# Kernel tuning notes

Measured on AMD Instinct MI355X. Metric: run time of the kernel, lower is better.

The kernel has to match this reference:

```python
import jax, jax.numpy as jnp
import numpy as np

N, D, E, EDGE_DIM, HID4 = 8192, 128, 262144, 50, 32


def setup_inputs() -> dict:
    key = jax.random.key(0)
    k = jax.random.split(key, 8)
    return {
        "mag": jax.random.uniform(k[0], (N, D), dtype=jnp.float32),
        "phase": jax.random.normal(k[1], (N, D), dtype=jnp.float32),
        "edge_index": jax.random.randint(k[2], (2, E), 0, N, dtype=jnp.int64),
        "rbf": jax.random.uniform(k[3], (E, EDGE_DIM), dtype=jnp.float32),
        "W1": jax.random.normal(k[4], (EDGE_DIM, HID4), dtype=jnp.float32) * 0.1,
        "b1": jnp.zeros((HID4,), dtype=jnp.float32),
        "W2": jax.random.normal(k[5], (HID4, 1), dtype=jnp.float32) * 0.1,
        "b2": jnp.zeros((1,), dtype=jnp.float32),
    }


def reference(mag, phase, edge_index, rbf, W1, b1, W2, b2):
    # score_ij = sum_d |z_i||z_j| cos(theta_i - theta_j) / sqrt(D)
    # cos(a-b) identity: = (mag*cos(phase)) @ (mag*cos(phase))^T + (mag*sin)@(mag*sin)^T
    scale = jnp.sqrt(jnp.asarray(mag.shape[-1], mag.dtype))
    a = mag * jnp.cos(phase)  # [N, D]
    b = mag * jnp.sin(phase)  # [N, D]
    scores = (a @ a.T + b @ b.T) / scale  # [N, N]
    # edge bias: Linear -> SiLU -> Linear -> scalar, scattered onto (i, j)
    h = jax.nn.silu(rbf @ W1 + b1)       # [E, HID4]
    bias = (h @ W2 + b2)[:, 0]           # [E]
    scores = scores.at[edge_index[0], edge_index[1]].add(bias)
    attn = jax.nn.softmax(scores, axis=1)  # softmax over keys j
    new_mag = attn @ mag
    new_phase = attn @ phase
    return new_mag, new_phase
```

## Files before the change

kernel.cpp:

```cpp
#include <hip/hip_runtime.h>
#include <hip/hip_bf16.h>

#define NN 8192
#define DD 128
#define DQK 256
#define EE 262144
#define EDGE_DIM 50
#define HID 32
#define CAP 96
#define SCALE 0.08838834764831845f
#define SCALE_LOG2E 0.12752455522410585f

using f32x4 = __attribute__((ext_vector_type(4))) float;
using f32x2 = __attribute__((ext_vector_type(2))) float;
using bf16x8 = __attribute__((ext_vector_type(8))) short;
using s16x4 = __attribute__((ext_vector_type(4))) short;

static __device__ __forceinline__ short f2b(float f) {
  __hip_bfloat16 h = __float2bfloat16(f);
  return __builtin_bit_cast(short, h);
}
static __device__ __forceinline__ float b2f(short s) {
  unsigned u = ((unsigned)(unsigned short)s) << 16;
  return __builtin_bit_cast(float, u);
}
static __device__ __forceinline__ void gll(const short* g, short* l) {
  __builtin_amdgcn_global_load_lds(
      (const __attribute__((address_space(1))) void*)g,
      (__attribute__((address_space(3))) void*)l, 16, 0, 0);
}

__global__ __launch_bounds__(256) void k1_mega(
    const float* __restrict__ mag, const float* __restrict__ phase,
    short* __restrict__ qkb, short* __restrict__ vtb, short* __restrict__ vb16,
    const float* __restrict__ rbf, const float* __restrict__ W1,
    const float* __restrict__ b1, const float* __restrict__ W2,
    const float* __restrict__ b2, const int* __restrict__ eidx,
    float* __restrict__ bias, int* __restrict__ cnt, int* __restrict__ slot) {
  __shared__ float tile[64][65];
  int b = blockIdx.x;
  int tid = threadIdx.x;
  if (b < 4096) {
    int t = b * 256 + tid;
    int n = t >> 7, d = t & 127;
    float m = mag[t], p = phase[t];
    float sn, cs;
    __sincosf(p, &sn, &cs);
    qkb[(size_t)n * DQK + d] = f2b(m * cs);
    qkb[(size_t)n * DQK + 128 + d] = f2b(m * sn);
    vb16[(size_t)n * DQK + d] = f2b(m);
    vb16[(size_t)n * DQK + 128 + d] = f2b(p);
    return;
  }
  if (b < 4608) {
    int r = b - 4096;
    int bn = r & 127, bd = (r >> 7) & 1, sel = r >> 8;
    const float* src = sel ? phase : mag;
#pragma unroll
    for (int rep = 0; rep < 16; ++rep) {
      int idx = rep * 256 + tid;
      int rr = idx >> 6, c = idx & 63;
      tile[rr][c] = src[(size_t)(bn * 64 + rr) * DD + bd * 64 + c];
    }
    __syncthreads();
#pragma unroll
    for (int rep = 0; rep < 16; ++rep) {
      int idx = rep * 256 + tid;
      int rr = idx >> 6, c = idx & 63;
      vtb[(size_t)(sel * 128 + bd * 64 + rr) * NN + bn * 64 + c] = f2b(tile[c][rr]);
    }
    return;
  }
  int e = (b - 4608) * 256 + tid;
  const float* rrow = rbf + (size_t)e * EDGE_DIM;
  f32x4 r4[12];
#pragma unroll
  for (int k = 0; k < 12; ++k) r4[k] = *reinterpret_cast<const f32x4*>(rrow + 4 * k);
  f32x2 rt2 = *reinterpret_cast<const f32x2*>(rrow + 48);
  float h[HID];
#pragma unroll
  for (int jj = 0; jj < HID; ++jj) h[jj] = b1[jj];
#pragma unroll
  for (int k = 0; k < 48; ++k) {
    float r = r4[k >> 2][k & 3];
#pragma unroll
    for (int jj = 0; jj < HID; ++jj) h[jj] += r * W1[k * HID + jj];
  }
#pragma unroll
  for (int jj = 0; jj < HID; ++jj)
    h[jj] += rt2.x * W1[48 * HID + jj] + rt2.y * W1[49 * HID + jj];
  float outv = b2[0];
#pragma unroll
  for (int jj = 0; jj < HID; ++jj) {
    float x = h[jj];
    outv += W2[jj] * (x / (1.0f + __expf(-x)));
  }
  bias[e] = outv;
  int i = eidx[e];
  int p = atomicAdd(&cnt[i], 1);
  if (p < CAP) slot[i * CAP + p] = e;
}

constexpr int TBM = 64;
constexpr int TBN = 128;

template <int NSPLIT>
__global__ __launch_bounds__(512, 4) void k5_flash(
    const short* __restrict__ qk,
    const short* __restrict__ vt,
    float* __restrict__ nump,
    float* __restrict__ denp) {
  constexpr int QCOLS = NN / NSPLIT;
  constexpr int NCHUNK = QCOLS / TBN;
  constexpr int GPQ = 8 / NSPLIT;
  __shared__ alignas(16) short Qs[TBM * 256];
  __shared__ alignas(16) short KV[2 * TBN * 64];
  __shared__ alignas(16) short Ps[TBM * 128];
  int b = blockIdx.x;
  int q = (b & 7) / GPQ;
  int rb = (b >> 3) * GPQ + (b & (GPQ - 1));
  int tid = threadIdx.x;
  int w = tid >> 6, lane = tid & 63;
  int wr = w >> 2, wc = w & 3;
  int l15 = lane & 15, quad = lane >> 4;
  int rsw = l15 & 7;
  int wbase = w * 64;
  int r0 = rb * TBM;
  int cbase = q * QCOLS;

#pragma unroll
  for (int p = 0; p < 4; ++p) {
    int idx = p * 512 + tid;
    int row = idx >> 5, gs = idx & 31;
    gll(qk + (size_t)(r0 + row) * DQK + ((gs ^ (row & 7)) * 8),
        &Qs[(p * 512 + wbase) * 8]);
  }

  f32x4 o[2][4] = {};
  float den[2][4] = {};
  __syncthreads();

  for (int ch = 0; ch < NCHUNK; ++ch) {
    int c0 = cbase + ch * TBN;
#pragma unroll
    for (int p = 0; p < 2; ++p) {
      int idx = p * 512 + tid;
      int col = idx >> 3, gs = idx & 7;
      gll(qk + (size_t)(c0 + col) * DQK + ((gs ^ (col & 7)) * 8),
          &KV[(p * 512 + wbase) * 8]);
    }
    __syncthreads();
    f32x4 s[2][2] = {};
#pragma unroll
    for (int bk = 0; bk < 4; ++bk) {
      int buf = bk & 1;
      if (bk < 3) {
        int nb = buf ^ 1;
#pragma unroll
        for (int p = 0; p < 2; ++p) {
          int idx = p * 512 + tid;
          int col = idx >> 3, gs = idx & 7;
          gll(qk + (size_t)(c0 + col) * DQK + (bk + 1) * 64 + ((gs ^ (col & 7)) * 8),
              &KV[nb * 8192 + (p * 512 + wbase) * 8]);
        }
      }
#pragma unroll
      for (int ks = 0; ks < 2; ++ks) {
        int g = ks * 4 + quad;
        bf16x8 a[2], bb[2];
#pragma unroll
        for (int rt = 0; rt < 2; ++rt)
          a[rt] = *(const bf16x8*)&Qs[(wr * 32 + rt * 16 + l15) * 256 +
                                      ((bk * 8 + g) ^ rsw) * 8];
#pragma unroll
        for (int ct = 0; ct < 2; ++ct)
          bb[ct] = *(const bf16x8*)&KV[buf * 8192 + (wc * 32 + ct * 16 + l15) * 64 +
                                       (g ^ rsw) * 8];
#pragma unroll
        for (int rt = 0; rt < 2; ++rt)
#pragma unroll
          for (int ct = 0; ct < 2; ++ct)
            s[rt][ct] = __builtin_amdgcn_mfma_f32_16x16x32_bf16(a[rt], bb[ct],
                                                                s[rt][ct], 0, 0, 0);
      }
      __syncthreads();
    }
#pragma unroll
    for (int rt = 0; rt < 2; ++rt)
#pragma unroll
      for (int ct = 0; ct < 2; ++ct) {
        int col = wc * 32 + ct * 16 + l15;
        int cg = col >> 3, co = col & 7;
#pragma unroll
        for (int r = 0; r < 4; ++r) {
          float pv = exp2f(s[rt][ct][r] * SCALE_LOG2E);
          den[rt][r] += pv;
          int row = wr * 32 + rt * 16 + quad * 4 + r;
          Ps[row * 128 + ((cg ^ (row & 7)) * 8 + co)] = f2b(pv);
        }
      }
    __syncthreads();
#pragma unroll
    for (int jb = 0; jb < 2; ++jb) {
#pragma unroll
      for (int p = 0; p < 4; ++p) {
        int idx = p * 512 + tid;
        int feat = idx >> 3, gs = idx & 7;
        gll(vt + (size_t)feat * NN + c0 + jb * 64 + ((gs ^ (feat & 7)) * 8),
            &KV[(p * 512 + wbase) * 8]);
      }
      __syncthreads();
#pragma unroll
      for (int ks = 0; ks < 2; ++ks) {
        int g = ks * 4 + quad;
        bf16x8 pa[2], vb[4];
#pragma unroll
        for (int rt = 0; rt < 2; ++rt) {
          int row = wr * 32 + rt * 16 + l15;
          pa[rt] = *(const bf16x8*)&Ps[row * 128 +
                                       (((jb * 8 + g) ^ (row & 7)) * 8)];
        }
#pragma unroll
        for (int ft = 0; ft < 4; ++ft)
          vb[ft] = *(const bf16x8*)&KV[(wc * 64 + ft * 16 + l15) * 64 + (g ^ rsw) * 8];
#pragma unroll
        for (int rt = 0; rt < 2; ++rt)
#pragma unroll
          for (int ft = 0; ft < 4; ++ft)
            o[rt][ft] = __builtin_amdgcn_mfma_f32_16x16x32_bf16(pa[rt], vb[ft],
                                                                o[rt][ft], 0, 0, 0);
      }
      __syncthreads();
    }
  }
  float* npB = nump + (size_t)q * NN * DQK;
#pragma unroll
  for (int rt = 0; rt < 2; ++rt)
#pragma unroll
    for (int ft = 0; ft < 4; ++ft) {
      int row = r0 + wr * 32 + rt * 16 + quad * 4;
      int feat = wc * 64 + ft * 16 + l15;
#pragma unroll
      for (int r = 0; r < 4; ++r)
        npB[(size_t)(row + r) * DQK + feat] = o[rt][ft][r];
    }
  float* dl = reinterpret_cast<float*>(KV);
#pragma unroll
  for (int rt = 0; rt < 2; ++rt)
#pragma unroll
    for (int r = 0; r < 4; ++r) {
      float d = den[rt][r];
      d += __shfl_xor(d, 1);
      d += __shfl_xor(d, 2);
      d += __shfl_xor(d, 4);
      d += __shfl_xor(d, 8);
      if (l15 == 0) dl[wc * TBM + wr * 32 + rt * 16 + quad * 4 + r] = d;
    }
  __syncthreads();
  if (tid < TBM) {
    float d = dl[0 * TBM + tid] + dl[1 * TBM + tid] + dl[2 * TBM + tid] +
              dl[3 * TBM + tid];
    denp[q * NN + r0 + tid] = d;
  }
}

__global__ __launch_bounds__(64) void k6_combine(
    const int* __restrict__ eidx, const float* __restrict__ bias,
    const int* __restrict__ cntArr, const int* __restrict__ slot,
    const short* __restrict__ qk, const short* __restrict__ vb16,
    const float* __restrict__ nump, const float* __restrict__ denp,
    float* __restrict__ out, int nsplit) {
  __shared__ short qs[DQK];
  __shared__ int js[CAP];
  __shared__ float bs[CAP];
  __shared__ float ess[CAP];
  __shared__ int keepf[CAP];
  __shared__ float ncl[2][32][8];
  __shared__ float dcl[2];
  int i = blockIdx.x;
  int lane = threadIdx.x;
  int cnt = cntArr[i];
  if (cnt > CAP) cnt = CAP;
  *reinterpret_cast<s16x4*>(&qs[lane * 4]) =
      *reinterpret_cast<const s16x4*>(qk + (size_t)i * DQK + lane * 4);
  for (int p = lane; p < cnt; p += 64) {
    int e = slot[i * CAP + p];
    js[p] = eidx[EE + e];
    bs[p] = bias[e];
  }
  __syncthreads();
  int sub = lane & 7;
  for (int p = lane >> 3; p < cnt; p += 8) {
    int j = js[p];
    const bf16x8* kb = reinterpret_cast<const bf16x8*>(qk + (size_t)j * DQK + sub * 32);
    const bf16x8* qa = reinterpret_cast<const bf16x8*>(qs + sub * 32);
    float sp = 0.f;
#pragma unroll
    for (int t = 0; t < 4; ++t) {
      bf16x8 qv = qa[t];
      bf16x8 kv = kb[t];
#pragma unroll
      for (int u = 0; u < 8; ++u) sp += b2f(qv[u]) * b2f(kv[u]);
    }
    sp += __shfl_xor(sp, 1);
    sp += __shfl_xor(sp, 2);
    sp += __shfl_xor(sp, 4);
    if (sub == 0) ess[p] = __expf(sp * SCALE);
  }
  __syncthreads();
  {
    int myp[2];
    float mybsum[2];
    int mykeep[2];
    int nm = 0;
    for (int p = lane; p < cnt; p += 64) {
      int j = js[p];
      float bsum = bs[p];
      int keep = 1;
      for (int qq = 0; qq < cnt; ++qq) {
        if (qq == p || js[qq] != j) continue;
        if (qq < p) { keep = 0; break; }
        bsum += bs[qq];
      }
      myp[nm] = p; mybsum[nm] = bsum; mykeep[nm] = keep; ++nm;
    }
    __syncthreads();
    for (int k = 0; k < nm; ++k) { bs[myp[k]] = mybsum[k]; keepf[myp[k]] = mykeep[k]; }
    __syncthreads();
  }
  int grp = lane >> 5;
  int l31 = lane & 31;
  f32x4 nc0 = {0.f, 0.f, 0.f, 0.f}, nc1 = {0.f, 0.f, 0.f, 0.f};
  float denc = 0.f;
  for (int p = grp; p < cnt; p += 2) {
    if (!keepf[p]) continue;
    float delta = ess[p] * expm1f(bs[p]);
    denc += delta;
    bf16x8 v = *reinterpret_cast<const bf16x8*>(vb16 + (size_t)js[p] * DQK + l31 * 8);
#pragma unroll
    for (int u = 0; u < 4; ++u) nc0[u] += delta * b2f(v[u]);
#pragma unroll
    for (int u = 0; u < 4; ++u) nc1[u] += delta * b2f(v[4 + u]);
  }
#pragma unroll
  for (int u = 0; u < 4; ++u) {
    ncl[grp][l31][u] = nc0[u];
    ncl[grp][l31][4 + u] = nc1[u];
  }
  if (l31 == 0) dcl[grp] = denc;
  __syncthreads();
  if (grp == 0) {
    float den = dcl[0] + dcl[1];
    f32x4 a0, a1;
#pragma unroll
    for (int u = 0; u < 4; ++u) {
      a0[u] = ncl[0][l31][u] + ncl[1][l31][u];
      a1[u] = ncl[0][l31][4 + u] + ncl[1][l31][4 + u];
    }
    for (int qq = 0; qq < nsplit; ++qq) {
      const float* np = nump + ((size_t)qq * NN + i) * DQK + l31 * 8;
      a0 += *reinterpret_cast<const f32x4*>(np);
      a1 += *reinterpret_cast<const f32x4*>(np + 4);
      den += denp[qq * NN + i];
    }
    float inv = 1.0f / den;
    a0 *= inv;
    a1 *= inv;
    float* dst = (l31 < 16) ? (out + (size_t)i * DD + l31 * 8)
                            : (out + (size_t)NN * DD + (size_t)i * DD + l31 * 8 - 128);
    *reinterpret_cast<f32x4*>(dst) = a0;
    *reinterpret_cast<f32x4*>(dst + 4) = a1;
  }
}

constexpr size_t OFF_QK = 0;
constexpr size_t OFF_VT = (size_t)NN * DQK * 2;
constexpr size_t OFF_VB16 = OFF_VT + (size_t)DQK * NN * 2;
constexpr size_t OFF_BIAS = OFF_VB16 + (size_t)NN * DQK * 2;
constexpr size_t OFF_CNT = OFF_BIAS + (size_t)EE * 4;
constexpr size_t OFF_SLOT = OFF_CNT + (size_t)NN * 4;
constexpr size_t OFF_NUMP = (OFF_SLOT + (size_t)NN * CAP * 4 + 255) & ~(size_t)255;
constexpr size_t WS_NEED4 = OFF_NUMP + 4ull * NN * DQK * 4 + 4ull * NN * 4;
constexpr size_t WS_NEED2 = OFF_NUMP + 2ull * NN * DQK * 4 + 2ull * NN * 4;

extern "C" void kernel_launch(void* const* d_in, const int* in_sizes, int n_in,
                              void* d_out, int out_size, void* d_ws, size_t ws_size,
                              hipStream_t stream) {
  const float* mag = (const float*)d_in[0];
  const float* phase = (const float*)d_in[1];
  const int* eidx = (const int*)d_in[2];
  const float* rbf = (const float*)d_in[3];
  const float* W1 = (const float*)d_in[4];
  const float* b1 = (const float*)d_in[5];
  const float* W2 = (const float*)d_in[6];
  const float* b2 = (const float*)d_in[7];
  float* out = (float*)d_out;
  char* ws = (char*)d_ws;
  if (ws_size < WS_NEED2) return;
  int nsplit = (ws_size >= WS_NEED4) ? 4 : 2;

  short* qkb = (short*)(ws + OFF_QK);
  short* vtb = (short*)(ws + OFF_VT);
  short* vb16 = (short*)(ws + OFF_VB16);
  float* bias = (float*)(ws + OFF_BIAS);
  int* cnt = (int*)(ws + OFF_CNT);
  int* slot = (int*)(ws + OFF_SLOT);
  float* nump = (float*)(ws + OFF_NUMP);
  float* denp = (float*)(ws + OFF_NUMP + (size_t)nsplit * NN * DQK * 4);

  hipMemsetAsync(cnt, 0, (size_t)NN * 4, stream);
  k1_mega<<<5632, 256, 0, stream>>>(mag, phase, qkb, vtb, vb16, rbf, W1, b1, W2,
                                    b2, eidx, bias, cnt, slot);
  if (nsplit == 4)
    k5_flash<4><<<(NN / TBM) * 4, 512, 0, stream>>>(qkb, vtb, nump, denp);
  else
    k5_flash<2><<<(NN / TBM) * 2, 512, 0, stream>>>(qkb, vtb, nump, denp);
  k6_combine<<<NN, 64, 0, stream>>>(eidx, bias, cnt, slot, qkb, vb16, nump, denp,
                                    out, nsplit);
}
```

Baseline: 268.0 us.

## Pipeline K and V staging across phases with fine-grained waitcnt and barriers

Restructures the flash-attention loop so K and V tiles are staged through a two-slot LDS ring: V halves are prefetched during the QK phase and the next chunk's first K slice is prefetched during PV. Full __syncthreads are replaced with explicit vmcnt waits and raw s_barrier, and MFMA sections are wrapped in s_setprio. The V tile is split into two 128-feature halves, which changes the output feature mapping. The aim is to hide global-to-LDS load latency behind compute, at the risk of subtle races from the hand-written waitcnt counts.

Measured after the change: 275.4 us. +2.7%, slower.

```diff
diff --git a/kernel.cpp b/kernel.cpp
--- a/kernel.cpp
+++ b/kernel.cpp
@@ -29,6 +29,10 @@
       (const __attribute__((address_space(1))) void*)g,
       (__attribute__((address_space(3))) void*)l, 16, 0, 0);
 }
+
+#define WAITV(N) asm volatile("s_waitcnt vmcnt(" #N ")" ::: "memory")
+#define WAITLGKM0() asm volatile("s_waitcnt lgkmcnt(0)" ::: "memory")
+#define BARX() asm volatile("s_barrier" ::: "memory")
 
 __global__ __launch_bounds__(256) void k1_mega(
     const float* __restrict__ mag, const float* __restrict__ phase,
@@ -114,7 +118,7 @@
   constexpr int NCHUNK = QCOLS / TBN;
   constexpr int GPQ = 8 / NSPLIT;
   __shared__ alignas(16) short Qs[TBM * 256];
-  __shared__ alignas(16) short KV[2 * TBN * 64];
+  __shared__ alignas(16) short KV[2 * 8192];
   __shared__ alignas(16) short Ps[TBM * 128];
   int b = blockIdx.x;
   int q = (b & 7) / GPQ;
@@ -128,6 +132,25 @@
   int r0 = rb * TBM;
   int cbase = q * QCOLS;
 
+  auto stageK = [&](int c0, int bk, int reg) {
+#pragma unroll
+    for (int p = 0; p < 2; ++p) {
+      int idx = p * 512 + tid;
+      int col = idx >> 3, gs = idx & 7;
+      gll(qk + (size_t)(c0 + col) * DQK + bk * 64 + ((gs ^ (col & 7)) * 8),
+          &KV[reg * 8192 + (p * 512 + wbase) * 8]);
+    }
+  };
+  auto stageV = [&](int c0, int jb, int h, int reg) {
+#pragma unroll
+    for (int p = 0; p < 2; ++p) {
+      int idx = p * 512 + tid;
+      int fl = idx >> 3, gs = idx & 7;
+      gll(vt + (size_t)(h * 128 + fl) * NN + c0 + jb * 64 + ((gs ^ (fl & 7)) * 8),
+          &KV[reg * 8192 + (p * 512 + wbase) * 8]);
+    }
+  };
+
 #pragma unroll
   for (int p = 0; p < 4; ++p) {
     int idx = p * 512 + tid;
@@ -135,35 +158,23 @@
     gll(qk + (size_t)(r0 + row) * DQK + ((gs ^ (row & 7)) * 8),
         &Qs[(p * 512 + wbase) * 8]);
   }
-
   f32x4 o[2][4] = {};
   float den[2][4] = {};
-  __syncthreads();
+  stageK(cbase, 0, 0);
+  WAITV(2);
+  BARX();
 
   for (int ch = 0; ch < NCHUNK; ++ch) {
     int c0 = cbase + ch * TBN;
-#pragma unroll
-    for (int p = 0; p < 2; ++p) {
-      int idx = p * 512 + tid;
-      int col = idx >> 3, gs = idx & 7;
-      gll(qk + (size_t)(c0 + col) * DQK + ((gs ^ (col & 7)) * 8),
-          &KV[(p * 512 + wbase) * 8]);
-    }
-    __syncthreads();
+    bool last = (ch == NCHUNK - 1);
     f32x4 s[2][2] = {};
 #pragma unroll
     for (int bk = 0; bk < 4; ++bk) {
-      int buf = bk & 1;
-      if (bk < 3) {
-        int nb = buf ^ 1;
-#pragma unroll
-        for (int p = 0; p < 2; ++p) {
-          int idx = p * 512 + tid;
-          int col = idx >> 3, gs = idx & 7;
-          gll(qk + (size_t)(c0 + col) * DQK + (bk + 1) * 64 + ((gs ^ (col & 7)) * 8),
-              &KV[nb * 8192 + (p * 512 + wbase) * 8]);
-        }
-      }
+      if (bk < 3) stageK(c0, bk + 1, (bk + 1) & 1);
+      else stageV(c0, 0, 0, 0);
+      WAITV(2);
+      BARX();
+      int reg = bk & 1;
 #pragma unroll
       for (int ks = 0; ks < 2; ++ks) {
         int g = ks * 4 + quad;
@@ -174,17 +185,21 @@
                                       ((bk * 8 + g) ^ rsw) * 8];
 #pragma unroll
         for (int ct = 0; ct < 2; ++ct)
-          bb[ct] = *(const bf16x8*)&KV[buf * 8192 + (wc * 32 + ct * 16 + l15) * 64 +
+          bb[ct] = *(const bf16x8*)&KV[reg * 8192 +
+                                       (wc * 32 + ct * 16 + l15) * 64 +
                                        (g ^ rsw) * 8];
+        __builtin_amdgcn_s_setprio(1);
 #pragma unroll
         for (int rt = 0; rt < 2; ++rt)
 #pragma unroll
           for (int ct = 0; ct < 2; ++ct)
             s[rt][ct] = __builtin_amdgcn_mfma_f32_16x16x32_bf16(a[rt], bb[ct],
                                                                 s[rt][ct], 0, 0, 0);
+        __builtin_amdgcn_s_setprio(0);
       }
-      __syncthreads();
-    }
+      BARX();
+    }
+    stageV(c0, 0, 1, 1);
 #pragma unroll
     for (int rt = 0; rt < 2; ++rt)
 #pragma unroll
@@ -199,38 +214,42 @@
           Ps[row * 128 + ((cg ^ (row & 7)) * 8 + co)] = f2b(pv);
         }
       }
-    __syncthreads();
-#pragma unroll
-    for (int jb = 0; jb < 2; ++jb) {
-#pragma unroll
-      for (int p = 0; p < 4; ++p) {
-        int idx = p * 512 + tid;
-        int feat = idx >> 3, gs = idx & 7;
-        gll(vt + (size_t)feat * NN + c0 + jb * 64 + ((gs ^ (feat & 7)) * 8),
-            &KV[(p * 512 + wbase) * 8]);
-      }
-      __syncthreads();
+    WAITLGKM0();
+    BARX();
+    bf16x8 pa[2][2];
+#pragma unroll
+    for (int v = 0; v < 4; ++v) {
+      int jb = v >> 1, h = v & 1, reg = v & 1;
+      if (v == 1) stageV(c0, 1, 0, 0);
+      else if (v == 2) stageV(c0, 1, 1, 1);
+      else if (v == 3 && !last) stageK(c0 + TBN, 0, 0);
+      if (v == 3 && last) { WAITV(0); } else { WAITV(2); }
+      BARX();
 #pragma unroll
       for (int ks = 0; ks < 2; ++ks) {
         int g = ks * 4 + quad;
-        bf16x8 pa[2], vb[4];
-#pragma unroll
-        for (int rt = 0; rt < 2; ++rt) {
-          int row = wr * 32 + rt * 16 + l15;
-          pa[rt] = *(const bf16x8*)&Ps[row * 128 +
-                                       (((jb * 8 + g) ^ (row & 7)) * 8)];
+        if (h == 0) {
+#pragma unroll
+          for (int rt = 0; rt < 2; ++rt)
+            pa[ks][rt] = *(const bf16x8*)&Ps[(wr * 32 + rt * 16 + l15) * 128 +
+                                             (((jb * 8 + g) ^ rsw) * 8)];
         }
-#pragma unroll
-        for (int ft = 0; ft < 4; ++ft)
-          vb[ft] = *(const bf16x8*)&KV[(wc * 64 + ft * 16 + l15) * 64 + (g ^ rsw) * 8];
+        bf16x8 vb[2];
+#pragma unroll
+        for (int ftl = 0; ftl < 2; ++ftl)
+          vb[ftl] = *(const bf16x8*)&KV[reg * 8192 +
+                                        (wc * 32 + ftl * 16 + l15) * 64 +
+                                        (g ^ rsw) * 8];
+        __builtin_amdgcn_s_setprio(1);
 #pragma unroll
         for (int rt = 0; rt < 2; ++rt)
 #pragma unroll
-          for (int ft = 0; ft < 4; ++ft)
-            o[rt][ft] = __builtin_amdgcn_mfma_f32_16x16x32_bf16(pa[rt], vb[ft],
-                                                                o[rt][ft], 0, 0, 0);
+          for (int ftl = 0; ftl < 2; ++ftl)
+            o[rt][h * 2 + ftl] = __builtin_amdgcn_mfma_f32_16x16x32_bf16(
+                pa[ks][rt], vb[ftl], o[rt][h * 2 + ftl], 0, 0, 0);
+        __builtin_amdgcn_s_setprio(0);
       }
-      __syncthreads();
+      BARX();
     }
   }
   float* npB = nump + (size_t)q * NN * DQK;
@@ -239,7 +258,7 @@
 #pragma unroll
     for (int ft = 0; ft < 4; ++ft) {
       int row = r0 + wr * 32 + rt * 16 + quad * 4;
-      int feat = wc * 64 + ft * 16 + l15;
+      int feat = (ft >> 1) * 128 + wc * 32 + (ft & 1) * 16 + l15;
 #pragma unroll
       for (int r = 0; r < 4; ++r)
         npB[(size_t)(row + r) * DQK + feat] = o[rt][ft][r];
```

## Load K and V fragments directly from global into registers, dropping LDS staging

Applied to the files above, without the earlier changes.

The flash kernel no longer stages K and V tiles through shared memory with async global-to-LDS copies. Each wave now loads its MFMA B-operand fragments straight from global memory into registers, double-buffered in software. This removes the KV shared buffer and most of the per-step barriers. In exchange, K/V data shared by the four row-waves is fetched redundantly from global/L2 instead of once per block, and latency hiding relies on register double-buffering.

After: 412.8 us. 54.0% more time.

```diff
diff --git a/kernel.cpp b/kernel.cpp
--- a/kernel.cpp
+++ b/kernel.cpp
@@ -114,8 +114,8 @@
   constexpr int NCHUNK = QCOLS / TBN;
   constexpr int GPQ = 8 / NSPLIT;
   __shared__ alignas(16) short Qs[TBM * 256];
-  __shared__ alignas(16) short KV[2 * TBN * 64];
   __shared__ alignas(16) short Ps[TBM * 128];
+  __shared__ float dl[4 * TBM];
   int b = blockIdx.x;
   int q = (b & 7) / GPQ;
   int rb = (b >> 3) * GPQ + (b & (GPQ - 1));
@@ -140,51 +140,45 @@
   float den[2][4] = {};
   __syncthreads();
 
+  const short* kbase = qk + (size_t)(cbase + wc * 32 + l15) * DQK + quad * 8;
+  const short* vbase = vt + (size_t)(wc * 64 + l15) * NN + cbase + quad * 8;
+
   for (int ch = 0; ch < NCHUNK; ++ch) {
-    int c0 = cbase + ch * TBN;
-#pragma unroll
-    for (int p = 0; p < 2; ++p) {
-      int idx = p * 512 + tid;
-      int col = idx >> 3, gs = idx & 7;
-      gll(qk + (size_t)(c0 + col) * DQK + ((gs ^ (col & 7)) * 8),
-          &KV[(p * 512 + wbase) * 8]);
-    }
-    __syncthreads();
     f32x4 s[2][2] = {};
-#pragma unroll
-    for (int bk = 0; bk < 4; ++bk) {
-      int buf = bk & 1;
-      if (bk < 3) {
-        int nb = buf ^ 1;
-#pragma unroll
-        for (int p = 0; p < 2; ++p) {
-          int idx = p * 512 + tid;
-          int col = idx >> 3, gs = idx & 7;
-          gll(qk + (size_t)(c0 + col) * DQK + (bk + 1) * 64 + ((gs ^ (col & 7)) * 8),
-              &KV[nb * 8192 + (p * 512 + wbase) * 8]);
-        }
-      }
+    bf16x8 kA[4], kB[4];
+    auto loadK = [&](bf16x8 (&kf)[4], int bk) {
+#pragma unroll
+      for (int ks = 0; ks < 2; ++ks)
+#pragma unroll
+        for (int ct = 0; ct < 2; ++ct)
+          kf[ks * 2 + ct] = *reinterpret_cast<const bf16x8*>(
+              kbase + (size_t)ch * (TBN * DQK) + ct * (16 * DQK) + bk * 64 +
+              ks * 32);
+    };
+    auto qkstep = [&](const bf16x8 (&kf)[4], int bk) {
 #pragma unroll
       for (int ks = 0; ks < 2; ++ks) {
-        int g = ks * 4 + quad;
-        bf16x8 a[2], bb[2];
+        bf16x8 a[2];
 #pragma unroll
         for (int rt = 0; rt < 2; ++rt)
           a[rt] = *(const bf16x8*)&Qs[(wr * 32 + rt * 16 + l15) * 256 +
-                                      ((bk * 8 + g) ^ rsw) * 8];
-#pragma unroll
-        for (int ct = 0; ct < 2; ++ct)
-          bb[ct] = *(const bf16x8*)&KV[buf * 8192 + (wc * 32 + ct * 16 + l15) * 64 +
-                                       (g ^ rsw) * 8];
+                                      ((bk * 8 + ks * 4 + quad) ^ rsw) * 8];
 #pragma unroll
         for (int rt = 0; rt < 2; ++rt)
 #pragma unroll
           for (int ct = 0; ct < 2; ++ct)
-            s[rt][ct] = __builtin_amdgcn_mfma_f32_16x16x32_bf16(a[rt], bb[ct],
-                                                                s[rt][ct], 0, 0, 0);
+            s[rt][ct] = __builtin_amdgcn_mfma_f32_16x16x32_bf16(
+                a[rt], kf[ks * 2 + ct], s[rt][ct], 0, 0, 0);
       }
-      __syncthreads();
-    }
+    };
+    loadK(kA, 0);
+    loadK(kB, 1);
+    qkstep(kA, 0);
+    loadK(kA, 2);
+    qkstep(kB, 1);
+    loadK(kB, 3);
+    qkstep(kA, 2);
+    qkstep(kB, 3);
 #pragma unroll
     for (int rt = 0; rt < 2; ++rt)
 #pragma unroll
@@ -200,38 +194,37 @@
         }
       }
     __syncthreads();
-#pragma unroll
-    for (int jb = 0; jb < 2; ++jb) {
-#pragma unroll
-      for (int p = 0; p < 4; ++p) {
-        int idx = p * 512 + tid;
-        int feat = idx >> 3, gs = idx & 7;
-        gll(vt + (size_t)feat * NN + c0 + jb * 64 + ((gs ^ (feat & 7)) * 8),
-            &KV[(p * 512 + wbase) * 8]);
+    bf16x8 vA[4], vB[4];
+    auto loadV = [&](bf16x8 (&vf)[4], int jb, int ks) {
+#pragma unroll
+      for (int ft = 0; ft < 4; ++ft)
+        vf[ft] = *reinterpret_cast<const bf16x8*>(
+            vbase + (size_t)ft * (16 * NN) + ch * TBN + jb * 64 + ks * 32);
+    };
+    auto pvstep = [&](const bf16x8 (&vf)[4], int jb, int ks) {
+      bf16x8 pa[2];
+#pragma unroll
+      for (int rt = 0; rt < 2; ++rt) {
+        int row = wr * 32 + rt * 16 + l15;
+        pa[rt] = *(const bf16x8*)&Ps[row * 128 +
+                                     (((jb * 8 + ks * 4 + quad) ^ (row & 7)) * 8)];
       }
-      __syncthreads();
-#pragma unroll
-      for (int ks = 0; ks < 2; ++ks) {
-        int g = ks * 4 + quad;
-        bf16x8 pa[2], vb[4];
-#pragma unroll
-        for (int rt = 0; rt < 2; ++rt) {
-          int row = wr * 32 + rt * 16 + l15;
-          pa[rt] = *(const bf16x8*)&Ps[row * 128 +
-                                       (((jb * 8 + g) ^ (row & 7)) * 8)];
-        }
+#pragma unroll
+      for (int rt = 0; rt < 2; ++rt)
 #pragma unroll
         for (int ft = 0; ft < 4; ++ft)
-          vb[ft] = *(const bf16x8*)&KV[(wc * 64 + ft * 16 + l15) * 64 + (g ^ rsw) * 8];
-#pragma unroll
-        for (int rt = 0; rt < 2; ++rt)
-#pragma unroll
-          for (int ft = 0; ft < 4; ++ft)
-            o[rt][ft] = __builtin_amdgcn_mfma_f32_16x16x32_bf16(pa[rt], vb[ft],
-                                                                o[rt][ft], 0, 0, 0);
-      }
-      __syncthreads();
-    }
+          o[rt][ft] = __builtin_amdgcn_mfma_f32_16x16x32_bf16(
+              pa[rt], vf[ft], o[rt][ft], 0, 0, 0);
+    };
+    loadV(vA, 0, 0);
+    loadV(vB, 0, 1);
+    pvstep(vA, 0, 0);
+    loadV(vA, 1, 0);
+    pvstep(vB, 0, 1);
+    loadV(vB, 1, 1);
+    pvstep(vA, 1, 0);
+    pvstep(vB, 1, 1);
+    __syncthreads();
   }
   float* npB = nump + (size_t)q * NN * DQK;
 #pragma unroll
@@ -244,7 +237,6 @@
       for (int r = 0; r < 4; ++r)
         npB[(size_t)(row + r) * DQK + feat] = o[rt][ft][r];
     }
-  float* dl = reinterpret_cast<float*>(KV);
 #pragma unroll
   for (int rt = 0; rt < 2; ++rt)
 #pragma unroll
```

## Transpose QK MFMA output, vectorize P stores, prefetch first V tile early

Applied to the files above, without the earlier changes.

The QK^T MFMA now runs with swapped operands, so each lane holds four consecutive key columns for a single query row. P values can then be packed into one 4-wide bf16 LDS store instead of four scalar stores, and the denominator reduction shrinks to two cross-quad shuffles. The first V-tile load is issued before the exp/P-write phase so its global latency overlaps with that work. One barrier per chunk is also removed. The layout change must keep the swizzle and row/column mapping exactly consistent, and a mistake there would silently corrupt the result.

Result: faster. 261.9 us (-2.3%).

```diff
diff --git a/kernel.cpp b/kernel.cpp
--- a/kernel.cpp
+++ b/kernel.cpp
@@ -137,7 +137,7 @@
   }
 
   f32x4 o[2][4] = {};
-  float den[2][4] = {};
+  float den[2] = {0.f, 0.f};
   __syncthreads();
 
   for (int ch = 0; ch < NCHUNK; ++ch) {
@@ -180,36 +180,49 @@
         for (int rt = 0; rt < 2; ++rt)
 #pragma unroll
           for (int ct = 0; ct < 2; ++ct)
-            s[rt][ct] = __builtin_amdgcn_mfma_f32_16x16x32_bf16(a[rt], bb[ct],
-                                                                s[rt][ct], 0, 0, 0);
+            s[ct][rt] = __builtin_amdgcn_mfma_f32_16x16x32_bf16(bb[ct], a[rt],
+                                                                s[ct][rt], 0, 0, 0);
       }
       __syncthreads();
     }
 #pragma unroll
-    for (int rt = 0; rt < 2; ++rt)
+    for (int p = 0; p < 4; ++p) {
+      int idx = p * 512 + tid;
+      int feat = idx >> 3, gs = idx & 7;
+      gll(vt + (size_t)feat * NN + c0 + ((gs ^ (feat & 7)) * 8),
+          &KV[(p * 512 + wbase) * 8]);
+    }
+#pragma unroll
+    for (int rt = 0; rt < 2; ++rt) {
+      int row = wr * 32 + rt * 16 + l15;
 #pragma unroll
       for (int ct = 0; ct < 2; ++ct) {
-        int col = wc * 32 + ct * 16 + l15;
-        int cg = col >> 3, co = col & 7;
+        s16x4 pk;
 #pragma unroll
         for (int r = 0; r < 4; ++r) {
-          float pv = exp2f(s[rt][ct][r] * SCALE_LOG2E);
-          den[rt][r] += pv;
-          int row = wr * 32 + rt * 16 + quad * 4 + r;
-          Ps[row * 128 + ((cg ^ (row & 7)) * 8 + co)] = f2b(pv);
+          float pv = exp2f(s[ct][rt][r] * SCALE_LOG2E);
+          den[rt] += pv;
+          pk[r] = f2b(pv);
         }
-      }
+        int cg = wc * 4 + ct * 2 + (quad >> 1);
+        *reinterpret_cast<s16x4*>(
+            &Ps[row * 128 + ((cg ^ (row & 7)) * 8 + (quad & 1) * 4)]) = pk;
+      }
+    }
     __syncthreads();
 #pragma unroll
     for (int jb = 0; jb < 2; ++jb) {
-#pragma unroll
-      for (int p = 0; p < 4; ++p) {
-        int idx = p * 512 + tid;
-        int feat = idx >> 3, gs = idx & 7;
-        gll(vt + (size_t)feat * NN + c0 + jb * 64 + ((gs ^ (feat & 7)) * 8),
-            &KV[(p * 512 + wbase) * 8]);
-      }
-      __syncthreads();
+      if (jb == 1) {
+        __syncthreads();
+#pragma unroll
+        for (int p = 0; p < 4; ++p) {
+          int idx = p * 512 + tid;
+          int feat = idx >> 3, gs = idx & 7;
+          gll(vt + (size_t)feat * NN + c0 + 64 + ((gs ^ (feat & 7)) * 8),
+              &KV[(p * 512 + wbase) * 8]);
+        }
+        __syncthreads();
+      }
 #pragma unroll
       for (int ks = 0; ks < 2; ++ks) {
         int g = ks * 4 + quad;
@@ -230,8 +243,8 @@
             o[rt][ft] = __builtin_amdgcn_mfma_f32_16x16x32_bf16(pa[rt], vb[ft],
                                                                 o[rt][ft], 0, 0, 0);
       }
-      __syncthreads();
-    }
+    }
+    __syncthreads();
   }
   float* npB = nump + (size_t)q * NN * DQK;
 #pragma unroll
@@ -246,16 +259,12 @@
     }
   float* dl = reinterpret_cast<float*>(KV);
 #pragma unroll
-  for (int rt = 0; rt < 2; ++rt)
-#pragma unroll
-    for (int r = 0; r < 4; ++r) {
-      float d = den[rt][r];
-      d += __shfl_xor(d, 1);
-      d += __shfl_xor(d, 2);
-      d += __shfl_xor(d, 4);
-      d += __shfl_xor(d, 8);
-      if (l15 == 0) dl[wc * TBM + wr * 32 + rt * 16 + quad * 4 + r] = d;
-    }
+  for (int rt = 0; rt < 2; ++rt) {
+    float d = den[rt];
+    d += __shfl_xor(d, 16);
+    d += __shfl_xor(d, 32);
+    if (lane < 16) dl[wc * TBM + wr * 32 + rt * 16 + lane] = d;
+  }
   __syncthreads();
   if (tid < TBM) {
     float d = dl[0 * TBM + tid] + dl[1 * TBM + tid] + dl[2 * TBM + tid] +
```
